# Optimization experiments

Measured on AMD Instinct MI355X. Metric: run time of the kernel, lower is better.

Reference implementation:

```python
import jax, jax.numpy as jnp
import numpy as np

IN_FEATURES = [32, 32]
OUT_FEATURES = [64, 64]
RANKS = [16, 16, 16, 16]


def _make_cores(key):
    dims = IN_FEATURES + OUT_FEATURES
    ranks = RANKS
    # init scale as in the torch module
    var = 2 ** (1.0 / len(dims)) / np.prod(np.power(np.array(ranks) + np.array(IN_FEATURES + IN_FEATURES), 1.0 / len(dims)))
    ub = float(np.sqrt(3.0 * var))
    ranks_ext = [ranks[-1]] + list(ranks)
    cores = []
    for i in range(len(dims)):
        key, k = jax.random.split(key)
        cores.append(jax.random.uniform(k, (ranks_ext[i], dims[i], ranks_ext[i + 1]), jnp.float32, -ub, ub))
    return cores, key


def setup_inputs() -> dict:
    key = jax.random.key(0)
    cores, key = _make_cores(key)
    key, kx, kb = jax.random.split(key, 3)
    x = jax.random.normal(kx, (8192, int(np.prod(IN_FEATURES))), jnp.float32)
    bias = jax.random.normal(kb, (int(np.prod(OUT_FEATURES)),), jnp.float32)
    return {"x": x, "core0": cores[0], "core1": cores[1], "core2": cores[2], "core3": cores[3], "bias": bias}


def reference(x, core0, core1, core2, core3, bias):
    # Tensor-ring contraction to build the dense weight, then linear.
    # core shapes: (16,32,16), (16,32,16), (16,64,16), (16,64,16)
    w = jnp.tensordot(core0, core1, axes=([2], [0]))        # (r, i0, i1, r)
    w = jnp.tensordot(w, core2, axes=([3], [0]))            # (r, i0, i1, o0, r)
    # last core: contract w's trailing rank with core axis 0 AND w's leading
    # rank with core's trailing rank (closes the ring) -> (i0, i1, o0, o1)
    w = jnp.tensordot(w, core3, axes=([4, 0], [0, 2]))
    d_out = int(np.prod(OUT_FEATURES))
    w = w.reshape(d_out, -1)                                # (4096, 1024)
    return x @ w.T + bias
```

## Files before the change

kernel.cpp:

```cpp
#include <hip/hip_runtime.h>
#include <hip/hip_bf16.h>
#include <stdint.h>

typedef unsigned short ushort_t;
typedef __attribute__((ext_vector_type(8))) short short8;
typedef __attribute__((ext_vector_type(4))) float floatx4;

__device__ __forceinline__ ushort_t f2bf(float f) {
    union { float f; unsigned u; } v; v.f = f;
    unsigned r = v.u + 0x7fffu + ((v.u >> 16) & 1u);
    return (ushort_t)(r >> 16);
}

__device__ __forceinline__ void async16(ushort_t* lds, const ushort_t* g) {
    __builtin_amdgcn_global_load_lds(
        (const __attribute__((address_space(1))) unsigned int*)g,
        (__attribute__((address_space(3))) unsigned int*)lds, 16, 0, 0);
}

__global__ __launch_bounds__(256) void prep_all(const float* __restrict__ x,
                                                const float* __restrict__ c0,
                                                const float* __restrict__ c1,
                                                const float* __restrict__ c2,
                                                const float* __restrict__ c3,
                                                ushort_t* __restrict__ Xb,
                                                ushort_t* __restrict__ A2b,
                                                ushort_t* __restrict__ Bg1) {
    const int b = blockIdx.x, t = threadIdx.x;
    if (b < 8192) {
        int i = b * 256 + t;
        float4 v = ((const float4*)x)[i];
        ushort4 r;
        r.x = f2bf(v.x); r.y = f2bf(v.y); r.z = f2bf(v.z); r.w = f2bf(v.w);
        ((ushort4*)Xb)[i] = r;
    } else if (b < 9216) {
        int id = (b - 8192) * 256 + t;
        int k = id & 255, ii = id >> 8;
        int r0 = k >> 4, r2 = k & 15;
        int i0 = ii >> 5, i1 = ii & 31;
        const float* p0 = c0 + (r0 * 32 + i0) * 16;
        const float* p1 = c1 + i1 * 16 + r2;
        float s = 0.f;
#pragma unroll
        for (int r1 = 0; r1 < 16; r1++) s += p0[r1] * p1[r1 * 512];
        A2b[id] = f2bf(s);
    } else {
        int id = (b - 9216) * 256 + t;
        int c = id & 1023, n = id >> 10;
        int bq = n >> 8, k = n & 255;
        int r0 = k >> 4, r2 = k & 15;
        int o0 = bq * 16 + (c >> 6), o1 = c & 63;
        const float* p2 = c2 + (r2 * 64 + o0) * 16;
        const float* p3 = c3 + o1 * 16 + r0;
        float s = 0.f;
#pragma unroll
        for (int r3 = 0; r3 < 16; r3++) s += p2[r3] * p3[r3 * 1024];
        Bg1[id] = f2bf(s);
    }
}

__global__ __launch_bounds__(256) void gemm1_u(const ushort_t* __restrict__ Xb,
                                               const ushort_t* __restrict__ Bg1,
                                               ushort_t* __restrict__ U) {
    __shared__ ushort_t As[128 * 32];
    __shared__ ushort_t Bs[128 * 32];
    const int t = threadIdx.x;
    const unsigned orig = blockIdx.x;
    const unsigned wg = (orig & 7) * 64 + (orig >> 3);
    const int row0 = (int)(wg >> 3) * 128;
    const int col0 = (int)(wg & 7) * 128;
    const int w = t >> 6, l = t & 63;
    const int wm = w >> 1, wn = w & 1;
    const int quad = l >> 4, ln = l & 15;

    floatx4 acc[4][4] = {};

    const ushort_t* aSrc = Xb  + (size_t)(row0 + (t >> 2)) * 1024 + (t & 3) * 8;
    const ushort_t* bSrc = Bg1 + (size_t)(col0 + (t >> 2)) * 1024 + (t & 3) * 8;

    for (int kk = 0; kk < 1024; kk += 32) {
        async16(&As[t * 8],        aSrc + kk);
        async16(&As[2048 + t * 8], aSrc + 64 * 1024 + kk);
        async16(&Bs[t * 8],        bSrc + kk);
        async16(&Bs[2048 + t * 8], bSrc + 64 * 1024 + kk);
        __syncthreads();

        short8 a[4], b[4];
#pragma unroll
        for (int ti = 0; ti < 4; ti++)
            a[ti] = *(const short8*)&As[(wm * 64 + ti * 16 + ln) * 32 + quad * 8];
#pragma unroll
        for (int tj = 0; tj < 4; tj++)
            b[tj] = *(const short8*)&Bs[(wn * 64 + tj * 16 + ln) * 32 + quad * 8];
#pragma unroll
        for (int ti = 0; ti < 4; ti++)
#pragma unroll
            for (int tj = 0; tj < 4; tj++)
                acc[ti][tj] = __builtin_amdgcn_mfma_f32_16x16x32_bf16(
                    a[ti], b[tj], acc[ti][tj], 0, 0, 0);
        __syncthreads();
    }

#pragma unroll
    for (int tj = 0; tj < 4; tj++) {
        const int n = col0 + wn * 64 + tj * 16 + ln;
#pragma unroll
        for (int ti = 0; ti < 4; ti++) {
            const int m = row0 + wm * 64 + ti * 16 + quad * 4;
#pragma unroll
            for (int r = 0; r < 4; r++)
                U[(size_t)(m + r) * 1024 + n] = f2bf(acc[ti][tj][r]);
        }
    }
}

__global__ __launch_bounds__(256) void gemm2_tr(const ushort_t* __restrict__ U,
                                                const ushort_t* __restrict__ A2b,
                                                const float* __restrict__ bias,
                                                float* __restrict__ out) {
    __shared__ ushort_t Us[4 * 128 * 32];
    const int t = threadIdx.x;
    const unsigned orig = blockIdx.x;
    const unsigned wg = (orig & 7) * 128 + (orig >> 3);
    const int jt = (int)(wg & 15), mt = (int)(wg >> 4);
    const int row0 = mt * 128;
    const int a0 = jt * 64;
    const int w = t >> 6, l = t & 63;
    const int wm = w >> 1, wn = w & 1;
    const int quad = l >> 4, ln = l & 15;

    short8 a2f[2][8];
#pragma unroll
    for (int tj = 0; tj < 2; tj++) {
        const ushort_t* ap = A2b + (size_t)(a0 + wn * 32 + tj * 16 + ln) * 256 + quad * 8;
#pragma unroll
        for (int s = 0; s < 8; s++)
            a2f[tj][s] = *(const short8*)&ap[s * 32];
    }

    floatx4 acc[4][4][2] = {};

    const ushort_t* uSrc = U + (size_t)(row0 + (t >> 2)) * 1024 + (t & 3) * 8;

#pragma unroll
    for (int kk8 = 0; kk8 < 8; kk8++) {
        const int kk = kk8 * 32;
#pragma unroll
        for (int b = 0; b < 4; b++) {
            async16(&Us[b * 4096 + t * 8],        uSrc + b * 256 + kk);
            async16(&Us[b * 4096 + 2048 + t * 8], uSrc + 64 * 1024 + b * 256 + kk);
        }
        __syncthreads();

#pragma unroll
        for (int b = 0; b < 4; b++) {
            short8 au[4];
#pragma unroll
            for (int ti = 0; ti < 4; ti++)
                au[ti] = *(const short8*)&Us[b * 4096 + (wm * 64 + ti * 16 + ln) * 32 + quad * 8];
#pragma unroll
            for (int ti = 0; ti < 4; ti++)
#pragma unroll
                for (int tj = 0; tj < 2; tj++)
                    acc[b][ti][tj] = __builtin_amdgcn_mfma_f32_16x16x32_bf16(
                        au[ti], a2f[tj][kk8], acc[b][ti][tj], 0, 0, 0);
        }
        __syncthreads();
    }

#pragma unroll
    for (int tj = 0; tj < 2; tj++) {
        const int a = a0 + wn * 32 + tj * 16 + ln;
        const float4 bv = ((const float4*)bias)[a];
#pragma unroll
        for (int ti = 0; ti < 4; ti++) {
            const int m = row0 + wm * 64 + ti * 16 + quad * 4;
#pragma unroll
            for (int r = 0; r < 4; r++) {
                float4 o;
                o.x = acc[0][ti][tj][r] + bv.x;
                o.y = acc[1][ti][tj][r] + bv.y;
                o.z = acc[2][ti][tj][r] + bv.z;
                o.w = acc[3][ti][tj][r] + bv.w;
                *(float4*)&out[(size_t)(m + r) * 4096 + (size_t)a * 4] = o;
            }
        }
    }
}

extern "C" void kernel_launch(void* const* d_in, const int* in_sizes, int n_in,
                              void* d_out, int out_size, void* d_ws, size_t ws_size,
                              hipStream_t stream) {
    const float* x    = (const float*)d_in[0];
    const float* c0   = (const float*)d_in[1];
    const float* c1   = (const float*)d_in[2];
    const float* c2   = (const float*)d_in[3];
    const float* c3   = (const float*)d_in[4];
    const float* bias = (const float*)d_in[5];
    float* out = (float*)d_out;

    char* ws = (char*)d_ws;
    ushort_t* Xb  = (ushort_t*)out;
    ushort_t* U   = (ushort_t*)ws;
    ushort_t* A2b = (ushort_t*)(ws + (16u << 20));
    ushort_t* Bg1 = (ushort_t*)(ws + (17u << 20));

    hipLaunchKernelGGL(prep_all, dim3(13312), dim3(256), 0, stream,
                       x, c0, c1, c2, c3, Xb, A2b, Bg1);
    hipLaunchKernelGGL(gemm1_u, dim3(512), dim3(256), 0, stream, Xb, Bg1, U);
    hipLaunchKernelGGL(gemm2_tr, dim3(1024), dim3(256), 0, stream, U, A2b, bias, out);
}
```

Before: 257.1 us.

## Drop LDS staging in both GEMMs, load MFMA fragments directly from global

Both GEMM kernels stop staging tiles in shared memory with async global-to-LDS copies and barriers. Each wave now loads its MFMA operand fragments straight from global memory, relying on L1/L2 for reuse across waves. gemm2 is also retiled so each block covers 32 output columns instead of 64, with each wave owning 32 rows, and the grid doubles to 2048 blocks. This removes barrier stalls and LDS traffic but gives up explicit cross-wave sharing, so global/L2 load traffic rises and the 16-byte-per-lane row-strided loads may coalesce poorly.

```diff
diff --git a/kernel.cpp b/kernel.cpp
--- a/kernel.cpp
+++ b/kernel.cpp
@@ -10,12 +10,6 @@
     union { float f; unsigned u; } v; v.f = f;
     unsigned r = v.u + 0x7fffu + ((v.u >> 16) & 1u);
     return (ushort_t)(r >> 16);
-}
-
-__device__ __forceinline__ void async16(ushort_t* lds, const ushort_t* g) {
-    __builtin_amdgcn_global_load_lds(
-        (const __attribute__((address_space(1))) unsigned int*)g,
-        (__attribute__((address_space(3))) unsigned int*)lds, 16, 0, 0);
 }
 
 __global__ __launch_bounds__(256) void prep_all(const float* __restrict__ x,
@@ -62,8 +56,6 @@
 __global__ __launch_bounds__(256) void gemm1_u(const ushort_t* __restrict__ Xb,
                                                const ushort_t* __restrict__ Bg1,
                                                ushort_t* __restrict__ U) {
-    __shared__ ushort_t As[128 * 32];
-    __shared__ ushort_t Bs[128 * 32];
     const int t = threadIdx.x;
     const unsigned orig = blockIdx.x;
     const unsigned wg = (orig & 7) * 64 + (orig >> 3);
@@ -75,30 +67,28 @@
 
     floatx4 acc[4][4] = {};
 
-    const ushort_t* aSrc = Xb  + (size_t)(row0 + (t >> 2)) * 1024 + (t & 3) * 8;
-    const ushort_t* bSrc = Bg1 + (size_t)(col0 + (t >> 2)) * 1024 + (t & 3) * 8;
+    const ushort_t* xp[4];
+    const ushort_t* gp[4];
+#pragma unroll
+    for (int ti = 0; ti < 4; ti++)
+        xp[ti] = Xb + (size_t)(row0 + wm * 64 + ti * 16 + ln) * 1024 + quad * 8;
+#pragma unroll
+    for (int tj = 0; tj < 4; tj++)
+        gp[tj] = Bg1 + (size_t)(col0 + wn * 64 + tj * 16 + ln) * 1024 + quad * 8;
 
+#pragma unroll 2
     for (int kk = 0; kk < 1024; kk += 32) {
-        async16(&As[t * 8],        aSrc + kk);
-        async16(&As[2048 + t * 8], aSrc + 64 * 1024 + kk);
-        async16(&Bs[t * 8],        bSrc + kk);
-        async16(&Bs[2048 + t * 8], bSrc + 64 * 1024 + kk);
-        __syncthreads();
-
         short8 a[4], b[4];
 #pragma unroll
-        for (int ti = 0; ti < 4; ti++)
-            a[ti] = *(const short8*)&As[(wm * 64 + ti * 16 + ln) * 32 + quad * 8];
+        for (int ti = 0; ti < 4; ti++) a[ti] = *(const short8*)&xp[ti][kk];
 #pragma unroll
-        for (int tj = 0; tj < 4; tj++)
-            b[tj] = *(const short8*)&Bs[(wn * 64 + tj * 16 + ln) * 32 + quad * 8];
+        for (int tj = 0; tj < 4; tj++) b[tj] = *(const short8*)&gp[tj][kk];
 #pragma unroll
         for (int ti = 0; ti < 4; ti++)
 #pragma unroll
             for (int tj = 0; tj < 4; tj++)
                 acc[ti][tj] = __builtin_amdgcn_mfma_f32_16x16x32_bf16(
                     a[ti], b[tj], acc[ti][tj], 0, 0, 0);
-        __syncthreads();
     }
 
 #pragma unroll
@@ -118,63 +108,56 @@
                                                 const ushort_t* __restrict__ A2b,
                                                 const float* __restrict__ bias,
                                                 float* __restrict__ out) {
-    __shared__ ushort_t Us[4 * 128 * 32];
     const int t = threadIdx.x;
     const unsigned orig = blockIdx.x;
-    const unsigned wg = (orig & 7) * 128 + (orig >> 3);
-    const int jt = (int)(wg & 15), mt = (int)(wg >> 4);
+    const unsigned wg = (orig & 7) * 256 + (orig >> 3);
+    const int jt = (int)(wg & 31), mt = (int)(wg >> 5);
     const int row0 = mt * 128;
-    const int a0 = jt * 64;
+    const int a0 = jt * 32;
     const int w = t >> 6, l = t & 63;
-    const int wm = w >> 1, wn = w & 1;
     const int quad = l >> 4, ln = l & 15;
+    const int mBase = row0 + w * 32;
 
     short8 a2f[2][8];
 #pragma unroll
     for (int tj = 0; tj < 2; tj++) {
-        const ushort_t* ap = A2b + (size_t)(a0 + wn * 32 + tj * 16 + ln) * 256 + quad * 8;
+        const ushort_t* ap = A2b + (size_t)(a0 + tj * 16 + ln) * 256 + quad * 8;
 #pragma unroll
         for (int s = 0; s < 8; s++)
             a2f[tj][s] = *(const short8*)&ap[s * 32];
     }
 
-    floatx4 acc[4][4][2] = {};
+    const ushort_t* up[2];
+#pragma unroll
+    for (int ti = 0; ti < 2; ti++)
+        up[ti] = U + (size_t)(mBase + ti * 16 + ln) * 1024 + quad * 8;
 
-    const ushort_t* uSrc = U + (size_t)(row0 + (t >> 2)) * 1024 + (t & 3) * 8;
+    floatx4 acc[4][2][2] = {};
 
 #pragma unroll
     for (int kk8 = 0; kk8 < 8; kk8++) {
-        const int kk = kk8 * 32;
 #pragma unroll
         for (int b = 0; b < 4; b++) {
-            async16(&Us[b * 4096 + t * 8],        uSrc + b * 256 + kk);
-            async16(&Us[b * 4096 + 2048 + t * 8], uSrc + 64 * 1024 + b * 256 + kk);
-        }
-        __syncthreads();
-
+            short8 au[2];
 #pragma unroll
-        for (int b = 0; b < 4; b++) {
-            short8 au[4];
+            for (int ti = 0; ti < 2; ti++)
+                au[ti] = *(const short8*)&up[ti][b * 256 + kk8 * 32];
 #pragma unroll
-            for (int ti = 0; ti < 4; ti++)
-                au[ti] = *(const short8*)&Us[b * 4096 + (wm * 64 + ti * 16 + ln) * 32 + quad * 8];
-#pragma unroll
-            for (int ti = 0; ti < 4; ti++)
+            for (int ti = 0; ti < 2; ti++)
 #pragma unroll
                 for (int tj = 0; tj < 2; tj++)
                     acc[b][ti][tj] = __builtin_amdgcn_mfma_f32_16x16x32_bf16(
                         au[ti], a2f[tj][kk8], acc[b][ti][tj], 0, 0, 0);
         }
-        __syncthreads();
     }
 
 #pragma unroll
     for (int tj = 0; tj < 2; tj++) {
-        const int a = a0 + wn * 32 + tj * 16 + ln;
+        const int a = a0 + tj * 16 + ln;
         const float4 bv = ((const float4*)bias)[a];
 #pragma unroll
-        for (int ti = 0; ti < 4; ti++) {
-            const int m = row0 + wm * 64 + ti * 16 + quad * 4;
+        for (int ti = 0; ti < 2; ti++) {
+            const int m = mBase + ti * 16 + quad * 4;
 #pragma unroll
             for (int r = 0; r < 4; r++) {
                 float4 o;
@@ -208,5 +191,5 @@
     hipLaunchKernelGGL(prep_all, dim3(13312), dim3(256), 0, stream,
                        x, c0, c1, c2, c3, Xb, A2b, Bg1);
     hipLaunchKernelGGL(gemm1_u, dim3(512), dim3(256), 0, stream, Xb, Bg1, U);
-    hipLaunchKernelGGL(gemm2_tr, dim3(1024), dim3(256), 0, stream, U, A2b, bias, out);
+    hipLaunchKernelGGL(gemm2_tr, dim3(2048), dim3(256), 0, stream, U, A2b, bias, out);
 }
```

Result: slower. 329.5 us (+28.2%).

## Double-buffer LDS tiles in both GEMMs and halve gemm2 row tile

Applied to the files above, without the earlier changes.

Both GEMM kernels now use two LDS buffers. The next K-slice's async global-to-LDS loads are issued before the MFMAs on the current slice, and one barrier per iteration is dropped, so load latency overlaps compute. gemm2 also shrinks its row tile from 128 to 64, doubling its grid to 2048 blocks and halving its accumulator registers, which should raise occupancy. The trade-off is more LDS per block in gemm1 and less reuse of the A2 fragments per block in gemm2.

```diff
diff --git a/kernel.cpp b/kernel.cpp
--- a/kernel.cpp
+++ b/kernel.cpp
@@ -62,8 +62,8 @@
 __global__ __launch_bounds__(256) void gemm1_u(const ushort_t* __restrict__ Xb,
                                                const ushort_t* __restrict__ Bg1,
                                                ushort_t* __restrict__ U) {
-    __shared__ ushort_t As[128 * 32];
-    __shared__ ushort_t Bs[128 * 32];
+    __shared__ ushort_t As[2][128 * 32];
+    __shared__ ushort_t Bs[2][128 * 32];
     const int t = threadIdx.x;
     const unsigned orig = blockIdx.x;
     const unsigned wg = (orig & 7) * 64 + (orig >> 3);
@@ -78,20 +78,26 @@
     const ushort_t* aSrc = Xb  + (size_t)(row0 + (t >> 2)) * 1024 + (t & 3) * 8;
     const ushort_t* bSrc = Bg1 + (size_t)(col0 + (t >> 2)) * 1024 + (t & 3) * 8;
 
-    for (int kk = 0; kk < 1024; kk += 32) {
-        async16(&As[t * 8],        aSrc + kk);
-        async16(&As[2048 + t * 8], aSrc + 64 * 1024 + kk);
-        async16(&Bs[t * 8],        bSrc + kk);
-        async16(&Bs[2048 + t * 8], bSrc + 64 * 1024 + kk);
-        __syncthreads();
+    async16(&As[0][t * 8],        aSrc);
+    async16(&As[0][2048 + t * 8], aSrc + 64 * 1024);
+    async16(&Bs[0][t * 8],        bSrc);
+    async16(&Bs[0][2048 + t * 8], bSrc + 64 * 1024);
+    __syncthreads();
+
+    int cur = 0;
+    for (int kk = 32; kk < 1024; kk += 32, cur ^= 1) {
+        async16(&As[cur ^ 1][t * 8],        aSrc + kk);
+        async16(&As[cur ^ 1][2048 + t * 8], aSrc + 64 * 1024 + kk);
+        async16(&Bs[cur ^ 1][t * 8],        bSrc + kk);
+        async16(&Bs[cur ^ 1][2048 + t * 8], bSrc + 64 * 1024 + kk);
 
         short8 a[4], b[4];
 #pragma unroll
         for (int ti = 0; ti < 4; ti++)
-            a[ti] = *(const short8*)&As[(wm * 64 + ti * 16 + ln) * 32 + quad * 8];
+            a[ti] = *(const short8*)&As[cur][(wm * 64 + ti * 16 + ln) * 32 + quad * 8];
 #pragma unroll
         for (int tj = 0; tj < 4; tj++)
-            b[tj] = *(const short8*)&Bs[(wn * 64 + tj * 16 + ln) * 32 + quad * 8];
+            b[tj] = *(const short8*)&Bs[cur][(wn * 64 + tj * 16 + ln) * 32 + quad * 8];
 #pragma unroll
         for (int ti = 0; ti < 4; ti++)
 #pragma unroll
@@ -100,6 +106,21 @@
                     a[ti], b[tj], acc[ti][tj], 0, 0, 0);
         __syncthreads();
     }
+    {
+        short8 a[4], b[4];
+#pragma unroll
+        for (int ti = 0; ti < 4; ti++)
+            a[ti] = *(const short8*)&As[cur][(wm * 64 + ti * 16 + ln) * 32 + quad * 8];
+#pragma unroll
+        for (int tj = 0; tj < 4; tj++)
+            b[tj] = *(const short8*)&Bs[cur][(wn * 64 + tj * 16 + ln) * 32 + quad * 8];
+#pragma unroll
+        for (int ti = 0; ti < 4; ti++)
+#pragma unroll
+            for (int tj = 0; tj < 4; tj++)
+                acc[ti][tj] = __builtin_amdgcn_mfma_f32_16x16x32_bf16(
+                    a[ti], b[tj], acc[ti][tj], 0, 0, 0);
+    }
 
 #pragma unroll
     for (int tj = 0; tj < 4; tj++) {
@@ -118,12 +139,12 @@
                                                 const ushort_t* __restrict__ A2b,
                                                 const float* __restrict__ bias,
                                                 float* __restrict__ out) {
-    __shared__ ushort_t Us[4 * 128 * 32];
+    __shared__ ushort_t Us[2][4][64 * 32];
     const int t = threadIdx.x;
     const unsigned orig = blockIdx.x;
-    const unsigned wg = (orig & 7) * 128 + (orig >> 3);
+    const unsigned wg = (orig & 7) * 256 + (orig >> 3);
     const int jt = (int)(wg & 15), mt = (int)(wg >> 4);
-    const int row0 = mt * 128;
+    const int row0 = mt * 64;
     const int a0 = jt * 64;
     const int w = t >> 6, l = t & 63;
     const int wm = w >> 1, wn = w & 1;
@@ -138,34 +159,48 @@
             a2f[tj][s] = *(const short8*)&ap[s * 32];
     }
 
-    floatx4 acc[4][4][2] = {};
+    floatx4 acc[4][2][2] = {};
 
     const ushort_t* uSrc = U + (size_t)(row0 + (t >> 2)) * 1024 + (t & 3) * 8;
 
 #pragma unroll
-    for (int kk8 = 0; kk8 < 8; kk8++) {
-        const int kk = kk8 * 32;
+    for (int b = 0; b < 4; b++)
+        async16(&Us[0][b][t * 8], uSrc + b * 256);
+    __syncthreads();
+
+    int cur = 0;
+#pragma unroll
+    for (int kk8 = 1; kk8 < 8; kk8++, cur ^= 1) {
+#pragma unroll
+        for (int b = 0; b < 4; b++)
+            async16(&Us[cur ^ 1][b][t * 8], uSrc + b * 256 + kk8 * 32);
 #pragma unroll
         for (int b = 0; b < 4; b++) {
-            async16(&Us[b * 4096 + t * 8],        uSrc + b * 256 + kk);
-            async16(&Us[b * 4096 + 2048 + t * 8], uSrc + 64 * 1024 + b * 256 + kk);
+            short8 au[2];
+#pragma unroll
+            for (int ti = 0; ti < 2; ti++)
+                au[ti] = *(const short8*)&Us[cur][b][(wm * 32 + ti * 16 + ln) * 32 + quad * 8];
+#pragma unroll
+            for (int ti = 0; ti < 2; ti++)
+#pragma unroll
+                for (int tj = 0; tj < 2; tj++)
+                    acc[b][ti][tj] = __builtin_amdgcn_mfma_f32_16x16x32_bf16(
+                        au[ti], a2f[tj][kk8 - 1], acc[b][ti][tj], 0, 0, 0);
         }
         __syncthreads();
-
-#pragma unroll
-        for (int b = 0; b < 4; b++) {
-            short8 au[4];
-#pragma unroll
-            for (int ti = 0; ti < 4; ti++)
-                au[ti] = *(const short8*)&Us[b * 4096 + (wm * 64 + ti * 16 + ln) * 32 + quad * 8];
-#pragma unroll
-            for (int ti = 0; ti < 4; ti++)
-#pragma unroll
-                for (int tj = 0; tj < 2; tj++)
-                    acc[b][ti][tj] = __builtin_amdgcn_mfma_f32_16x16x32_bf16(
-                        au[ti], a2f[tj][kk8], acc[b][ti][tj], 0, 0, 0);
-        }
-        __syncthreads();
+    }
+#pragma unroll
+    for (int b = 0; b < 4; b++) {
+        short8 au[2];
+#pragma unroll
+        for (int ti = 0; ti < 2; ti++)
+            au[ti] = *(const short8*)&Us[cur][b][(wm * 32 + ti * 16 + ln) * 32 + quad * 8];
+#pragma unroll
+        for (int ti = 0; ti < 2; ti++)
+#pragma unroll
+            for (int tj = 0; tj < 2; tj++)
+                acc[b][ti][tj] = __builtin_amdgcn_mfma_f32_16x16x32_bf16(
+                    au[ti], a2f[tj][7], acc[b][ti][tj], 0, 0, 0);
     }
 
 #pragma unroll
@@ -173,8 +208,8 @@
         const int a = a0 + wn * 32 + tj * 16 + ln;
         const float4 bv = ((const float4*)bias)[a];
 #pragma unroll
-        for (int ti = 0; ti < 4; ti++) {
-            const int m = row0 + wm * 64 + ti * 16 + quad * 4;
+        for (int ti = 0; ti < 2; ti++) {
+            const int m = row0 + wm * 32 + ti * 16 + quad * 4;
 #pragma unroll
             for (int r = 0; r < 4; r++) {
                 float4 o;
@@ -208,5 +243,5 @@
     hipLaunchKernelGGL(prep_all, dim3(13312), dim3(256), 0, stream,
                        x, c0, c1, c2, c3, Xb, A2b, Bg1);
     hipLaunchKernelGGL(gemm1_u, dim3(512), dim3(256), 0, stream, Xb, Bg1, U);
-    hipLaunchKernelGGL(gemm2_tr, dim3(1024), dim3(256), 0, stream, U, A2b, bias, out);
-}
+    hipLaunchKernelGGL(gemm2_tr, dim3(2048), dim3(256), 0, stream, U, A2b, bias, out);
+}
```

Result: faster. 245.9 us (-4.4%).
